# Kernel optimization log

Measured on AMD Instinct MI355X. Metric: run time of the kernel, lower is better.

## Reference

```python
import jax, jax.numpy as jnp
import numpy as np

DIM = 256
HEADS = 8
QUERY_IDX = 0


def setup_inputs() -> dict:
    key = jax.random.key(0)
    ks = jax.random.split(key, 9)
    B, N, D = 32, 8192, DIM
    s = 0.02
    return {
        "x": jax.random.normal(ks[0], (B, N, D), dtype=jnp.float32),
        "Wq": jax.random.normal(ks[1], (D, D), dtype=jnp.float32) * s,
        "bq": jnp.zeros((D,), dtype=jnp.float32),
        "Wk": jax.random.normal(ks[2], (D, D), dtype=jnp.float32) * s,
        "bk": jnp.zeros((D,), dtype=jnp.float32),
        "Wv": jax.random.normal(ks[3], (D, D), dtype=jnp.float32) * s,
        "bv": jnp.zeros((D,), dtype=jnp.float32),
        "Wo": jax.random.normal(ks[4], (D, D), dtype=jnp.float32) * s,
        "bo": jnp.zeros((D,), dtype=jnp.float32),
    }


def reference(x, Wq, bq, Wk, bk, Wv, bv, Wo, bo):
    B, N, D = x.shape
    H = HEADS
    dh = D // H
    scale = 1.0 / np.sqrt(dh)
    # single-token query slice [B, 1, D]
    q = jax.lax.dynamic_slice_in_dim(x, QUERY_IDX, 1, axis=1)
    Q = (q @ Wq + bq).reshape(B, 1, H, dh)
    K = (x @ Wk + bk).reshape(B, N, H, dh)
    V = (x @ Wv + bv).reshape(B, N, H, dh)
    # decode-style attention: one query vs N keys per head
    scores = jnp.einsum("bqhd,bkhd->bhqk", Q, K) * scale  # [B,H,1,N]
    w = jax.nn.softmax(scores, axis=-1)
    attn = jnp.einsum("bhqk,bkhd->bqhd", w, V).reshape(B, 1, D)
    residual = attn @ Wo + bo
    return q + residual
```

## Files before the change

### kernel.cpp

```cpp
#include <hip/hip_runtime.h>


namespace {
constexpr int DIMC = 256;
constexpr int NHEAD = 8;
constexpr int NTOKENS = 8192;
constexpr int NBATCH = 32;
constexpr int TOK_PER_BLOCK = 128;
constexpr int CHUNKS = NTOKENS / TOK_PER_BLOCK;
constexpr float SCALE = 0.17677669529663687f;

constexpr int WS_SCTX = 0;
constexpr int WS_L    = NBATCH * NHEAD * DIMC;
constexpr int WS_QK   = WS_L + NBATCH * NHEAD;
constexpr int WS_QB   = WS_QK + NBATCH * NHEAD * DIMC;
constexpr int WS_PART = WS_QB + NBATCH * NHEAD;
constexpr size_t WS_NEEDED_BYTES =
    (size_t)(WS_PART + NBATCH * CHUNKS * NHEAD * DIMC) * 4;
}

template <int CTRL>
__device__ __forceinline__ float dppmov(float v) {
  return __int_as_float(
      __builtin_amdgcn_update_dpp(0, __float_as_int(v), CTRL, 0xF, 0xF, true));
}
template <int PAT>
__device__ __forceinline__ float swzf(float v) {
  return __int_as_float(__builtin_amdgcn_ds_swizzle(__float_as_int(v), PAT));
}

__global__ __launch_bounds__(256) void k1_prep(
    const float* __restrict__ x, const float* __restrict__ Wq,
    const float* __restrict__ bq, const float* __restrict__ Wk,
    const float* __restrict__ bk, float* __restrict__ qk_g,
    float* __restrict__ qb_g, float* __restrict__ sctx_g,
    float* __restrict__ l_g) {
  const int b = blockIdx.x, tid = threadIdx.x;
  __shared__ float xs[DIMC];
  __shared__ float Qs[DIMC];
  xs[tid] = x[(size_t)b * NTOKENS * DIMC + tid];
#pragma unroll
  for (int r = 0; r < NHEAD; ++r) sctx_g[b * NHEAD * DIMC + r * DIMC + tid] = 0.f;
  if (tid < NHEAD) l_g[b * NHEAD + tid] = 0.f;
  __syncthreads();
  float acc = bq[tid];
#pragma unroll 4
  for (int d = 0; d < DIMC; ++d) acc += xs[d] * Wq[d * DIMC + tid];
  Qs[tid] = acc;
  __syncthreads();
#pragma unroll
  for (int h = 0; h < NHEAD; ++h) {
    float s = 0.f;
#pragma unroll
    for (int j = 0; j < 32; ++j) s += Qs[h * 32 + j] * Wk[tid * DIMC + h * 32 + j];
    qk_g[b * NHEAD * DIMC + h * DIMC + tid] = s;
  }
  if (tid < NHEAD) {
    float s = 0.f;
#pragma unroll
    for (int j = 0; j < 32; ++j) s += Qs[tid * 32 + j] * bk[tid * 32 + j];
    qb_g[b * NHEAD + tid] = s;
  }
}

template <bool PARTIAL>
__global__ __launch_bounds__(256) void k2_attn(
    const float* __restrict__ x, const float* __restrict__ qk_g,
    const float* __restrict__ qb_g, float* __restrict__ dst_g,
    float* __restrict__ l_g) {
  const int b = blockIdx.x >> 6;
  const int chunk = blockIdx.x & (CHUNKS - 1);
  const int tid = threadIdx.x;
  const int wave = tid >> 6;
  const int lane = tid & 63;
  const int q2 = lane & 3;

  const float4* qkp = (const float4*)(qk_g + b * NHEAD * DIMC);
  float4 qk[8];
#pragma unroll
  for (int h = 0; h < 8; ++h) qk[h] = qkp[h * 64 + lane];
  const float qba = qb_g[b * 8 + q2];
  const float qbb = qb_g[b * 8 + 4 + q2];

  float4 sc[8];
#pragma unroll
  for (int j = 0; j < 8; ++j) sc[j] = make_float4(0.f, 0.f, 0.f, 0.f);
  float laccA = 0.f, laccB = 0.f;

  const int n0 = chunk * TOK_PER_BLOCK + wave * 32;
  const float4* xp = (const float4*)(x + (size_t)b * NTOKENS * DIMC);
  float4 xv = xp[(size_t)n0 * 64 + lane];
  for (int t = 0; t < 32; ++t) {
    const int tn = (t + 1) & 31;
    float4 xn = xp[(size_t)(n0 + tn) * 64 + lane];

    float p[8];
#pragma unroll
    for (int h = 0; h < 8; ++h)
      p[h] = xv.x * qk[h].x + xv.y * qk[h].y + xv.z * qk[h].z + xv.w * qk[h].w;
#pragma unroll
    for (int h = 0; h < 8; ++h) {
      p[h] += dppmov<0xB1>(p[h]);
      p[h] += dppmov<0x4E>(p[h]);
    }
    const bool c0 = (lane & 1) != 0, c1 = (lane & 2) != 0;
    float t0 = c0 ? p[1] : p[0], t1 = c0 ? p[3] : p[2];
    float s0 = c0 ? p[5] : p[4], s1 = c0 ? p[7] : p[6];
    float va = c1 ? t1 : t0;
    float vb = c1 ? s1 : s0;
    va += swzf<0x101F>(va); vb += swzf<0x101F>(vb);
    va += dppmov<0x128>(va); vb += dppmov<0x128>(vb);
    va += swzf<0x401F>(va); vb += swzf<0x401F>(vb);
    va += __shfl_xor(va, 32, 64); vb += __shfl_xor(vb, 32, 64);

    const float ea = __expf((va + qba) * SCALE);
    const float eb = __expf((vb + qbb) * SCALE);
    laccA += ea; laccB += eb;

    float r[8];
    r[0] = ea; r[1] = dppmov<0xB1>(ea);
    r[2] = dppmov<0x4E>(ea); r[3] = dppmov<0x4E>(r[1]);
    r[4] = eb; r[5] = dppmov<0xB1>(eb);
    r[6] = dppmov<0x4E>(eb); r[7] = dppmov<0x4E>(r[5]);
#pragma unroll
    for (int j = 0; j < 8; ++j) {
      sc[j].x += r[j] * xv.x; sc[j].y += r[j] * xv.y;
      sc[j].z += r[j] * xv.z; sc[j].w += r[j] * xv.w;
    }
    xv = xn;
  }

  if constexpr (PARTIAL) {
    __shared__ float4 red[2][8][64];
    if (wave >= 2) {
#pragma unroll
      for (int j = 0; j < 8; ++j) red[wave - 2][j][lane] = sc[j];
    }
    __syncthreads();
    if (wave < 2) {
#pragma unroll
      for (int j = 0; j < 8; ++j) {
        float4 v = red[wave][j][lane];
        sc[j].x += v.x; sc[j].y += v.y; sc[j].z += v.z; sc[j].w += v.w;
      }
    }
    __syncthreads();
    if (wave == 1) {
#pragma unroll
      for (int j = 0; j < 8; ++j) red[0][j][lane] = sc[j];
    }
    __syncthreads();
    if (wave == 0) {
      float4* pp = (float4*)dst_g + ((size_t)(b * CHUNKS + chunk) * 8) * 64 + lane;
#pragma unroll
      for (int j = 0; j < 8; ++j) {
        float4 v = red[0][j][lane];
        sc[j].x += v.x; sc[j].y += v.y; sc[j].z += v.z; sc[j].w += v.w;
        pp[j * 64] = sc[j];
      }
    }
  } else {
    float* sb = dst_g + b * NHEAD * DIMC;
    const int dbase = lane * 4;
#pragma unroll
    for (int j = 0; j < 8; ++j) {
      const int h = (j < 4) ? (q2 ^ j) : (4 + (q2 ^ (j - 4)));
      atomicAdd(&sb[h * DIMC + dbase + 0], sc[j].x);
      atomicAdd(&sb[h * DIMC + dbase + 1], sc[j].y);
      atomicAdd(&sb[h * DIMC + dbase + 2], sc[j].z);
      atomicAdd(&sb[h * DIMC + dbase + 3], sc[j].w);
    }
  }

  if (lane < 4) {
    atomicAdd(&l_g[b * 8 + lane], laccA);
    atomicAdd(&l_g[b * 8 + 4 + lane], laccB);
  }
}

__global__ __launch_bounds__(128) void k2b_reduce(
    const float4* __restrict__ part, float* __restrict__ sctx_g) {
  const int gid = blockIdx.x * 128 + threadIdx.x;
  const int lane = gid & 63;
  const int j = (gid >> 6) & 7;
  const int b = gid >> 9;
  const float4* p = part + ((size_t)b * CHUNKS * 8 + j) * 64 + lane;
  float4 acc = make_float4(0.f, 0.f, 0.f, 0.f);
  for (int c = 0; c < CHUNKS; ++c) {
    float4 v = p[(size_t)c * 8 * 64];
    acc.x += v.x; acc.y += v.y; acc.z += v.z; acc.w += v.w;
  }
  const int q2 = lane & 3;
  const int h = (j < 4) ? (q2 ^ j) : (4 + (q2 ^ (j - 4)));
  float4* dst = (float4*)(sctx_g + (b * NHEAD + h) * DIMC) + lane;
  *dst = acc;
}

__global__ __launch_bounds__(256) void k3_final(
    const float* __restrict__ x, const float* __restrict__ Wv,
    const float* __restrict__ bv, const float* __restrict__ Wo,
    const float* __restrict__ bo, const float* __restrict__ sctx_g,
    const float* __restrict__ l_g, float* __restrict__ out) {
  const int b = blockIdx.x, tid = threadIdx.x;
  __shared__ float ctxs[NHEAD * DIMC];
  __shared__ float os[DIMC];
  __shared__ float ls[NHEAD];
#pragma unroll
  for (int r = 0; r < NHEAD; ++r)
    ctxs[r * DIMC + tid] = sctx_g[b * NHEAD * DIMC + r * DIMC + tid];
  if (tid < NHEAD) ls[tid] = l_g[b * NHEAD + tid];
  __syncthreads();
  const int h = tid >> 5;
  float s = 0.f;
#pragma unroll 4
  for (int d = 0; d < DIMC; ++d) s += ctxs[h * DIMC + d] * Wv[d * DIMC + tid];
  const float o = s / ls[h] + bv[tid];
  os[tid] = o;
  __syncthreads();
  float acc = bo[tid] + x[(size_t)b * NTOKENS * DIMC + tid];
#pragma unroll 4
  for (int j = 0; j < DIMC; ++j) acc += os[j] * Wo[j * DIMC + tid];
  out[b * DIMC + tid] = acc;
}

extern "C" void kernel_launch(void* const* d_in, const int* in_sizes, int n_in,
                              void* d_out, int out_size, void* d_ws, size_t ws_size,
                              hipStream_t stream) {
  const float* x  = (const float*)d_in[0];
  const float* Wq = (const float*)d_in[1];
  const float* bq = (const float*)d_in[2];
  const float* Wk = (const float*)d_in[3];
  const float* bk = (const float*)d_in[4];
  const float* Wv = (const float*)d_in[5];
  const float* bv = (const float*)d_in[6];
  const float* Wo = (const float*)d_in[7];
  const float* bo = (const float*)d_in[8];
  float* ws = (float*)d_ws;
  float* sctx = ws + WS_SCTX;
  float* lg   = ws + WS_L;
  float* qk   = ws + WS_QK;
  float* qb   = ws + WS_QB;
  float* part = ws + WS_PART;

  k1_prep<<<NBATCH, 256, 0, stream>>>(x, Wq, bq, Wk, bk, qk, qb, sctx, lg);
  if (ws_size >= WS_NEEDED_BYTES) {
    k2_attn<true><<<NBATCH * CHUNKS, 256, 0, stream>>>(x, qk, qb, part, lg);
    k2b_reduce<<<NBATCH * NHEAD * 64 / 128, 128, 0, stream>>>((const float4*)part,
                                                              sctx);
  } else {
    k2_attn<false><<<NBATCH * CHUNKS, 256, 0, stream>>>(x, qk, qb, sctx, lg);
  }
  k3_final<<<NBATCH, 256, 0, stream>>>(x, Wv, bv, Wo, bo, sctx, lg,
                                       (float*)d_out);
}
```

Baseline: 495.9 us.

## Batch 8-token loads in attention, fuse partial reduce into final, stage Wk in LDS

The attention kernel now loads x in groups of 8 tokens, double-buffered, and batches the cross-lane reductions and exps across those tokens. This raises memory-level parallelism and instruction-level parallelism in the bandwidth-bound main pass, at the cost of more registers. The separate partial-reduce kernel is removed and folded into the final kernel, saving one launch. The prep kernel stages transposed Wk tiles in padded LDS to coalesce loads, folds SCALE into qk and qb, and the GEMV loops use split accumulators.

```diff
diff --git a/kernel.cpp b/kernel.cpp
--- a/kernel.cpp
+++ b/kernel.cpp
@@ -38,28 +38,47 @@
   const int b = blockIdx.x, tid = threadIdx.x;
   __shared__ float xs[DIMC];
   __shared__ float Qs[DIMC];
+  __shared__ float wk[DIMC][33];
   xs[tid] = x[(size_t)b * NTOKENS * DIMC + tid];
 #pragma unroll
   for (int r = 0; r < NHEAD; ++r) sctx_g[b * NHEAD * DIMC + r * DIMC + tid] = 0.f;
   if (tid < NHEAD) l_g[b * NHEAD + tid] = 0.f;
   __syncthreads();
-  float acc = bq[tid];
-#pragma unroll 4
-  for (int d = 0; d < DIMC; ++d) acc += xs[d] * Wq[d * DIMC + tid];
-  Qs[tid] = acc;
+  {
+    float a0 = bq[tid], a1 = 0.f, a2 = 0.f, a3 = 0.f;
+#pragma unroll 8
+    for (int d = 0; d < DIMC; d += 4) {
+      a0 += xs[d + 0] * Wq[(d + 0) * DIMC + tid];
+      a1 += xs[d + 1] * Wq[(d + 1) * DIMC + tid];
+      a2 += xs[d + 2] * Wq[(d + 2) * DIMC + tid];
+      a3 += xs[d + 3] * Wq[(d + 3) * DIMC + tid];
+    }
+    Qs[tid] = (a0 + a1) + (a2 + a3);
+  }
   __syncthreads();
-#pragma unroll
   for (int h = 0; h < NHEAD; ++h) {
-    float s = 0.f;
-#pragma unroll
-    for (int j = 0; j < 32; ++j) s += Qs[h * 32 + j] * Wk[tid * DIMC + h * 32 + j];
-    qk_g[b * NHEAD * DIMC + h * DIMC + tid] = s;
+#pragma unroll
+    for (int kk = 0; kk < 32; ++kk) {
+      const int i = kk * 256 + tid;
+      wk[i >> 5][i & 31] = Wk[(size_t)(i >> 5) * DIMC + h * 32 + (i & 31)];
+    }
+    __syncthreads();
+    float s0 = 0.f, s1 = 0.f, s2 = 0.f, s3 = 0.f;
+#pragma unroll
+    for (int j = 0; j < 32; j += 4) {
+      s0 += Qs[h * 32 + j + 0] * wk[tid][j + 0];
+      s1 += Qs[h * 32 + j + 1] * wk[tid][j + 1];
+      s2 += Qs[h * 32 + j + 2] * wk[tid][j + 2];
+      s3 += Qs[h * 32 + j + 3] * wk[tid][j + 3];
+    }
+    qk_g[b * NHEAD * DIMC + h * DIMC + tid] = SCALE * ((s0 + s1) + (s2 + s3));
+    __syncthreads();
   }
   if (tid < NHEAD) {
     float s = 0.f;
 #pragma unroll
     for (int j = 0; j < 32; ++j) s += Qs[tid * 32 + j] * bk[tid * 32 + j];
-    qb_g[b * NHEAD + tid] = s;
+    qb_g[b * NHEAD + tid] = SCALE * s;
   }
 }
 
@@ -74,6 +93,7 @@
   const int wave = tid >> 6;
   const int lane = tid & 63;
   const int q2 = lane & 3;
+  const bool c0 = (lane & 1) != 0, c1 = (lane & 2) != 0;
 
   const float4* qkp = (const float4*)(qk_g + b * NHEAD * DIMC);
   float4 qk[8];
@@ -89,45 +109,71 @@
 
   const int n0 = chunk * TOK_PER_BLOCK + wave * 32;
   const float4* xp = (const float4*)(x + (size_t)b * NTOKENS * DIMC);
-  float4 xv = xp[(size_t)n0 * 64 + lane];
-  for (int t = 0; t < 32; ++t) {
-    const int tn = (t + 1) & 31;
-    float4 xn = xp[(size_t)(n0 + tn) * 64 + lane];
-
-    float p[8];
-#pragma unroll
-    for (int h = 0; h < 8; ++h)
-      p[h] = xv.x * qk[h].x + xv.y * qk[h].y + xv.z * qk[h].z + xv.w * qk[h].w;
-#pragma unroll
-    for (int h = 0; h < 8; ++h) {
-      p[h] += dppmov<0xB1>(p[h]);
-      p[h] += dppmov<0x4E>(p[h]);
-    }
-    const bool c0 = (lane & 1) != 0, c1 = (lane & 2) != 0;
-    float t0 = c0 ? p[1] : p[0], t1 = c0 ? p[3] : p[2];
-    float s0 = c0 ? p[5] : p[4], s1 = c0 ? p[7] : p[6];
-    float va = c1 ? t1 : t0;
-    float vb = c1 ? s1 : s0;
-    va += swzf<0x101F>(va); vb += swzf<0x101F>(vb);
-    va += dppmov<0x128>(va); vb += dppmov<0x128>(vb);
-    va += swzf<0x401F>(va); vb += swzf<0x401F>(vb);
-    va += __shfl_xor(va, 32, 64); vb += __shfl_xor(vb, 32, 64);
-
-    const float ea = __expf((va + qba) * SCALE);
-    const float eb = __expf((vb + qbb) * SCALE);
-    laccA += ea; laccB += eb;
-
-    float r[8];
-    r[0] = ea; r[1] = dppmov<0xB1>(ea);
-    r[2] = dppmov<0x4E>(ea); r[3] = dppmov<0x4E>(r[1]);
-    r[4] = eb; r[5] = dppmov<0xB1>(eb);
-    r[6] = dppmov<0x4E>(eb); r[7] = dppmov<0x4E>(r[5]);
-#pragma unroll
-    for (int j = 0; j < 8; ++j) {
-      sc[j].x += r[j] * xv.x; sc[j].y += r[j] * xv.y;
-      sc[j].z += r[j] * xv.z; sc[j].w += r[j] * xv.w;
-    }
-    xv = xn;
+
+  float4 xa[8], xb[8];
+#pragma unroll
+  for (int u = 0; u < 8; ++u) xa[u] = xp[(size_t)(n0 + u) * 64 + lane];
+
+#pragma unroll 1
+  for (int g = 0; g < 4; ++g) {
+    if (g < 3) {
+      const int n1 = n0 + (g + 1) * 8;
+#pragma unroll
+      for (int u = 0; u < 8; ++u) xb[u] = xp[(size_t)(n1 + u) * 64 + lane];
+    }
+    float va[8], vb[8];
+#pragma unroll
+    for (int u = 0; u < 8; ++u) {
+      float p[8];
+#pragma unroll
+      for (int h = 0; h < 8; ++h)
+        p[h] = xa[u].x * qk[h].x + xa[u].y * qk[h].y + xa[u].z * qk[h].z +
+               xa[u].w * qk[h].w;
+#pragma unroll
+      for (int h = 0; h < 8; ++h) {
+        p[h] += dppmov<0xB1>(p[h]);
+        p[h] += dppmov<0x4E>(p[h]);
+      }
+      float t0 = c0 ? p[1] : p[0], t1 = c0 ? p[3] : p[2];
+      float s0 = c0 ? p[5] : p[4], s1 = c0 ? p[7] : p[6];
+      va[u] = c1 ? t1 : t0;
+      vb[u] = c1 ? s1 : s0;
+    }
+#pragma unroll
+    for (int u = 0; u < 8; ++u) { va[u] += swzf<0x101F>(va[u]); vb[u] += swzf<0x101F>(vb[u]); }
+#pragma unroll
+    for (int u = 0; u < 8; ++u) { va[u] += dppmov<0x128>(va[u]); vb[u] += dppmov<0x128>(vb[u]); }
+#pragma unroll
+    for (int u = 0; u < 8; ++u) { va[u] += swzf<0x401F>(va[u]); vb[u] += swzf<0x401F>(vb[u]); }
+#pragma unroll
+    for (int u = 0; u < 8; ++u) { va[u] += __shfl_xor(va[u], 32, 64); vb[u] += __shfl_xor(vb[u], 32, 64); }
+    float ea[8], eb[8];
+#pragma unroll
+    for (int u = 0; u < 8; ++u) {
+      ea[u] = __expf(va[u] + qba);
+      eb[u] = __expf(vb[u] + qbb);
+      laccA += ea[u];
+      laccB += eb[u];
+    }
+#pragma unroll
+    for (int u = 0; u < 8; ++u) {
+      float r0 = ea[u], r1 = dppmov<0xB1>(ea[u]);
+      float r2 = dppmov<0x4E>(ea[u]), r3 = dppmov<0x4E>(r1);
+      float r4 = eb[u], r5 = dppmov<0xB1>(eb[u]);
+      float r6 = dppmov<0x4E>(eb[u]), r7 = dppmov<0x4E>(r5);
+      sc[0].x += r0 * xa[u].x; sc[0].y += r0 * xa[u].y; sc[0].z += r0 * xa[u].z; sc[0].w += r0 * xa[u].w;
+      sc[1].x += r1 * xa[u].x; sc[1].y += r1 * xa[u].y; sc[1].z += r1 * xa[u].z; sc[1].w += r1 * xa[u].w;
+      sc[2].x += r2 * xa[u].x; sc[2].y += r2 * xa[u].y; sc[2].z += r2 * xa[u].z; sc[2].w += r2 * xa[u].w;
+      sc[3].x += r3 * xa[u].x; sc[3].y += r3 * xa[u].y; sc[3].z += r3 * xa[u].z; sc[3].w += r3 * xa[u].w;
+      sc[4].x += r4 * xa[u].x; sc[4].y += r4 * xa[u].y; sc[4].z += r4 * xa[u].z; sc[4].w += r4 * xa[u].w;
+      sc[5].x += r5 * xa[u].x; sc[5].y += r5 * xa[u].y; sc[5].z += r5 * xa[u].z; sc[5].w += r5 * xa[u].w;
+      sc[6].x += r6 * xa[u].x; sc[6].y += r6 * xa[u].y; sc[6].z += r6 * xa[u].z; sc[6].w += r6 * xa[u].w;
+      sc[7].x += r7 * xa[u].x; sc[7].y += r7 * xa[u].y; sc[7].z += r7 * xa[u].z; sc[7].w += r7 * xa[u].w;
+    }
+    if (g < 3) {
+#pragma unroll
+      for (int u = 0; u < 8; ++u) xa[u] = xb[u];
+    }
   }
 
   if constexpr (PARTIAL) {
@@ -178,49 +224,63 @@
   }
 }
 
-__global__ __launch_bounds__(128) void k2b_reduce(
-    const float4* __restrict__ part, float* __restrict__ sctx_g) {
-  const int gid = blockIdx.x * 128 + threadIdx.x;
-  const int lane = gid & 63;
-  const int j = (gid >> 6) & 7;
-  const int b = gid >> 9;
-  const float4* p = part + ((size_t)b * CHUNKS * 8 + j) * 64 + lane;
-  float4 acc = make_float4(0.f, 0.f, 0.f, 0.f);
-  for (int c = 0; c < CHUNKS; ++c) {
-    float4 v = p[(size_t)c * 8 * 64];
-    acc.x += v.x; acc.y += v.y; acc.z += v.z; acc.w += v.w;
-  }
-  const int q2 = lane & 3;
-  const int h = (j < 4) ? (q2 ^ j) : (4 + (q2 ^ (j - 4)));
-  float4* dst = (float4*)(sctx_g + (b * NHEAD + h) * DIMC) + lane;
-  *dst = acc;
-}
-
+template <bool FROMPART>
 __global__ __launch_bounds__(256) void k3_final(
     const float* __restrict__ x, const float* __restrict__ Wv,
     const float* __restrict__ bv, const float* __restrict__ Wo,
-    const float* __restrict__ bo, const float* __restrict__ sctx_g,
+    const float* __restrict__ bo, const float* __restrict__ src,
     const float* __restrict__ l_g, float* __restrict__ out) {
   const int b = blockIdx.x, tid = threadIdx.x;
-  __shared__ float ctxs[NHEAD * DIMC];
+  __shared__ float ctxs[NHEAD * 260];
   __shared__ float os[DIMC];
   __shared__ float ls[NHEAD];
-#pragma unroll
-  for (int r = 0; r < NHEAD; ++r)
-    ctxs[r * DIMC + tid] = sctx_g[b * NHEAD * DIMC + r * DIMC + tid];
   if (tid < NHEAD) ls[tid] = l_g[b * NHEAD + tid];
+  if constexpr (FROMPART) {
+    const int lane = tid & 63, j = tid >> 6, q2 = lane & 3;
+    const float4* p0 =
+        (const float4*)src + ((size_t)(b * CHUNKS) * 8 + j) * 64 + lane;
+    float4 a0 = make_float4(0.f, 0.f, 0.f, 0.f);
+    float4 a1 = make_float4(0.f, 0.f, 0.f, 0.f);
+    for (int c = 0; c < CHUNKS; ++c) {
+      float4 v0 = p0[(size_t)c * 512];
+      float4 v1 = p0[(size_t)c * 512 + 256];
+      a0.x += v0.x; a0.y += v0.y; a0.z += v0.z; a0.w += v0.w;
+      a1.x += v1.x; a1.y += v1.y; a1.z += v1.z; a1.w += v1.w;
+    }
+    const int h0 = q2 ^ j, h1 = 4 + (q2 ^ j);
+    *(float4*)&ctxs[h0 * 260 + lane * 4] = a0;
+    *(float4*)&ctxs[h1 * 260 + lane * 4] = a1;
+  } else {
+#pragma unroll
+    for (int r = 0; r < NHEAD; ++r)
+      ctxs[r * 260 + tid] = src[b * NHEAD * DIMC + r * DIMC + tid];
+  }
   __syncthreads();
   const int h = tid >> 5;
-  float s = 0.f;
-#pragma unroll 4
-  for (int d = 0; d < DIMC; ++d) s += ctxs[h * DIMC + d] * Wv[d * DIMC + tid];
-  const float o = s / ls[h] + bv[tid];
-  os[tid] = o;
+  {
+    float s0 = 0.f, s1 = 0.f, s2 = 0.f, s3 = 0.f;
+#pragma unroll 8
+    for (int d = 0; d < DIMC; d += 4) {
+      s0 += ctxs[h * 260 + d + 0] * Wv[(d + 0) * DIMC + tid];
+      s1 += ctxs[h * 260 + d + 1] * Wv[(d + 1) * DIMC + tid];
+      s2 += ctxs[h * 260 + d + 2] * Wv[(d + 2) * DIMC + tid];
+      s3 += ctxs[h * 260 + d + 3] * Wv[(d + 3) * DIMC + tid];
+    }
+    os[tid] = ((s0 + s1) + (s2 + s3)) / ls[h] + bv[tid];
+  }
   __syncthreads();
-  float acc = bo[tid] + x[(size_t)b * NTOKENS * DIMC + tid];
-#pragma unroll 4
-  for (int j = 0; j < DIMC; ++j) acc += os[j] * Wo[j * DIMC + tid];
-  out[b * DIMC + tid] = acc;
+  {
+    float a0 = bo[tid] + x[(size_t)b * NTOKENS * DIMC + tid];
+    float a1 = 0.f, a2 = 0.f, a3 = 0.f;
+#pragma unroll 8
+    for (int j = 0; j < DIMC; j += 4) {
+      a0 += os[j + 0] * Wo[(j + 0) * DIMC + tid];
+      a1 += os[j + 1] * Wo[(j + 1) * DIMC + tid];
+      a2 += os[j + 2] * Wo[(j + 2) * DIMC + tid];
+      a3 += os[j + 3] * Wo[(j + 3) * DIMC + tid];
+    }
+    out[b * DIMC + tid] = (a0 + a1) + (a2 + a3);
+  }
 }
 
 extern "C" void kernel_launch(void* const* d_in, const int* in_sizes, int n_in,
@@ -245,11 +305,11 @@
   k1_prep<<<NBATCH, 256, 0, stream>>>(x, Wq, bq, Wk, bk, qk, qb, sctx, lg);
   if (ws_size >= WS_NEEDED_BYTES) {
     k2_attn<true><<<NBATCH * CHUNKS, 256, 0, stream>>>(x, qk, qb, part, lg);
-    k2b_reduce<<<NBATCH * NHEAD * 64 / 128, 128, 0, stream>>>((const float4*)part,
-                                                              sctx);
+    k3_final<true><<<NBATCH, 256, 0, stream>>>(x, Wv, bv, Wo, bo, part, lg,
+                                               (float*)d_out);
   } else {
     k2_attn<false><<<NBATCH * CHUNKS, 256, 0, stream>>>(x, qk, qb, sctx, lg);
-  }
-  k3_final<<<NBATCH, 256, 0, stream>>>(x, Wv, bv, Wo, bo, sctx, lg,
-                                       (float*)d_out);
-}
+    k3_final<false><<<NBATCH, 256, 0, stream>>>(x, Wv, bv, Wo, bo, sctx, lg,
+                                                (float*)d_out);
+  }
+}
```

Result: faster. 455.9 us (-8.1%).
